# Kernel optimization log

Measured on AMD Instinct MI355X. Metric: run time of the kernel, lower is better.

## Reference

```python
import jax, jax.numpy as jnp
import numpy as np
from jax import lax

B, T1, T2, C = 8, 128, 128, 256
K = 3

def setup_inputs() -> dict:
    key = jax.random.key(0)
    k1, k2, kw, kb = jax.random.split(key, 4)
    x1 = jax.random.normal(k1, (B, T1, C), dtype=jnp.float32)
    x2 = jax.random.normal(k2, (B, T2, C), dtype=jnp.float32)
    # conv2d: in_channels = 2C, out_channels = C, kernel 3x3 (OIHW)
    fan_in = 2 * C * K * K
    bound = 1.0 / np.sqrt(fan_in)
    W = jax.random.uniform(kw, (C, 2 * C, K, K), jnp.float32, -bound, bound)
    b = jax.random.uniform(kb, (C,), jnp.float32, -bound, bound)
    alpha = jnp.float32(0.5)
    return {"x1": x1, "x2": x2, "W": W, "b": b, "alpha": alpha}


def reference(x1, x2, W, b, alpha):
    # x1: [B, T1, C], x2: [B, T2, C]
    a = jnp.transpose(x1, (0, 2, 1))  # [B, C, T1]
    c2 = jnp.transpose(x2, (0, 2, 1))  # [B, C, T2]
    Bd, Cd, T1d = a.shape
    T2d = c2.shape[-1]
    # joint outer-product tensor: [B, 2C, T1, T2]
    j1 = jnp.broadcast_to(a[:, :, :, None], (Bd, Cd, T1d, T2d))
    j2 = jnp.broadcast_to(c2[:, :, None, :], (Bd, Cd, T1d, T2d))
    joint = jnp.concatenate([j1, j2], axis=1)
    out = lax.conv_general_dilated(
        joint, W, window_strides=(1, 1), padding="SAME",
        dimension_numbers=("NCHW", "OIHW", "NCHW"))
    out = out + b[None, :, None, None]
    out = jax.nn.gelu(out, approximate=False)  # torch nn.GELU default = exact erf
    out_T1 = jnp.mean(out, axis=-1)            # [B, C, T1]
    out_T1 = jnp.transpose(out_T1, (0, 2, 1))  # [B, T1, C]
    return out_T1 * alpha + x1
```

## Files before the change

kernel.cpp:

```cpp
#include <hip/hip_runtime.h>
#include <math.h>

#define B_   8
#define T_   128
#define C_   256
#define XLDS 264
#define WLDP 136

typedef unsigned short ushort;
typedef ushort ushort8v __attribute__((ext_vector_type(8)));
typedef __bf16 bf16x8  __attribute__((ext_vector_type(8)));
typedef float  f32x4   __attribute__((ext_vector_type(4)));

__device__ __forceinline__ ushort f2bf(float f) {
    unsigned u = __float_as_uint(f);
    u += 0x7fffu + ((u >> 16) & 1u);
    return (ushort)(u >> 16);
}

__device__ __forceinline__ float gelu_fast(float x) {
    float x2 = x * x;
    float y2 = x * fmaf(-0.10294234f, x2, -2.30220818f);
    float e  = __builtin_amdgcn_exp2f(y2);
    return x * __builtin_amdgcn_rcpf(1.0f + e);
}

__global__ __launch_bounds__(256) void tc_pack(
    const float* __restrict__ x1, const float* __restrict__ x2,
    const float* __restrict__ W, ushort* __restrict__ Xp,
    ushort* __restrict__ Wt)
{
    const int bid = blockIdx.x, t = threadIdx.x;
    if (bid < 256) {
        __shared__ ushort lw[4608];
        const float* src = W + (size_t)bid * 4608;
        #pragma unroll
        for (int i = 0; i < 18; ++i)
            lw[t + i * 256] = f2bf(src[t + i * 256]);
        __syncthreads();
        #pragma unroll
        for (int i = 0; i < 18; ++i) {
            int d  = t + i * 256;
            int s  = d / 2304;
            int e  = d - s * 2304;
            int nj = e / 768;
            int k  = e - nj * 768;
            int sh = k >> 8, ci = k & 255;
            ushort v = (s == 0) ? lw[ci * 9 + sh * 3 + nj]
                                : lw[(256 + ci) * 9 + nj * 3 + sh];
            Wt[((size_t)s * 768 + bid * 3 + nj) * 768 + k] = v;
        }
    } else {
        int g = (bid - 256) * 256 + t;
        int e = g * 8;
        int s  = e >> 18;
        int me = e & 262143;
        const float* src = (s ? x2 : x1) + me;
        float4 lo = *(const float4*)src;
        float4 hi = *(const float4*)(src + 4);
        ushort8v u;
        u[0] = f2bf(lo.x); u[1] = f2bf(lo.y); u[2] = f2bf(lo.z); u[3] = f2bf(lo.w);
        u[4] = f2bf(hi.x); u[5] = f2bf(hi.y); u[6] = f2bf(hi.z); u[7] = f2bf(hi.w);
        *(ushort8v*)&Xp[e] = u;
    }
}

__global__ __launch_bounds__(256, 3) void tc_gemm(
    const ushort* __restrict__ Xp, const ushort* __restrict__ Wt,
    float* __restrict__ AB)
{
    __shared__ ushort Xs[66 * XLDS];
    __shared__ ushort Ws[64 * WLDP];

    const int tn = blockIdx.x;
    const int tm = blockIdx.y;
    const int s  = blockIdx.z;
    const int u  = threadIdx.x;
    const int l  = u & 63, w = u >> 6;
    const int wr = w >> 1, wc = w & 1;
    const int r16 = l & 15, kb = l >> 4;

    const int b_     = tm >> 1;
    const int t_base = (tm & 1) * 64;
    const ushort* Xb = Xp + ((size_t)s * 1024 + b_ * T_) * C_;
    const ushort* Wb = Wt + ((size_t)s * 768 + tn * 64) * 768;

    {
        ushort8v zero = {};
        #pragma unroll
        for (int j = 0; j < 9; ++j) {
            int c = u + j * 256;
            if (j < 8 || c < 2112) {
                int i  = c >> 5;
                int kc = (c & 31) * 8;
                int t  = t_base + i - 1;
                ushort8v v = (t >= 0 && t < T_)
                           ? *(const ushort8v*)(Xb + (size_t)t * C_ + kc) : zero;
                *(ushort8v*)&Xs[i * XLDS + kc] = v;
            }
        }
    }

    ushort8v wbuf[4];
    #pragma unroll
    for (int j = 0; j < 4; ++j) {
        int c = u + j * 256;
        wbuf[j] = *(const ushort8v*)(Wb + (size_t)(c >> 4) * 768 + (c & 15) * 8);
    }

    f32x4 acc[2][2] = {};
    #pragma unroll
    for (int r = 0; r < 6; ++r) {
        const int sh = r >> 1, p = r & 1;
        __syncthreads();
        #pragma unroll
        for (int j = 0; j < 4; ++j) {
            int c = u + j * 256;
            *(ushort8v*)&Ws[(c >> 4) * WLDP + (c & 15) * 8] = wbuf[j];
        }
        if (r < 5) {
            const int rn = r + 1;
            const ushort* wsrc = Wb + (rn >> 1) * 256 + (rn & 1) * 128;
            #pragma unroll
            for (int j = 0; j < 4; ++j) {
                int c = u + j * 256;
                wbuf[j] = *(const ushort8v*)(wsrc + (size_t)(c >> 4) * 768 + (c & 15) * 8);
            }
        }
        __syncthreads();
        #pragma unroll
        for (int ks = 0; ks < 4; ++ks) {
            const int ka = p * 128 + ks * 32 + kb * 8;
            const int kw_ = ks * 32 + kb * 8;
            bf16x8 a0 = __builtin_bit_cast(bf16x8,
                *(const ushort8v*)&Xs[(wr * 32 + r16 + sh) * XLDS + ka]);
            bf16x8 a1 = __builtin_bit_cast(bf16x8,
                *(const ushort8v*)&Xs[(wr * 32 + 16 + r16 + sh) * XLDS + ka]);
            bf16x8 b0 = __builtin_bit_cast(bf16x8,
                *(const ushort8v*)&Ws[(wc * 32 + r16) * WLDP + kw_]);
            bf16x8 b1 = __builtin_bit_cast(bf16x8,
                *(const ushort8v*)&Ws[(wc * 32 + 16 + r16) * WLDP + kw_]);
            acc[0][0] = __builtin_amdgcn_mfma_f32_16x16x32_bf16(a0, b0, acc[0][0], 0, 0, 0);
            acc[0][1] = __builtin_amdgcn_mfma_f32_16x16x32_bf16(a0, b1, acc[0][1], 0, 0, 0);
            acc[1][0] = __builtin_amdgcn_mfma_f32_16x16x32_bf16(a1, b0, acc[1][0], 0, 0, 0);
            acc[1][1] = __builtin_amdgcn_mfma_f32_16x16x32_bf16(a1, b1, acc[1][1], 0, 0, 0);
        }
    }

    #pragma unroll
    for (int j = 0; j < 2; ++j) {
        int n = tn * 64 + wc * 32 + j * 16 + r16;
        #pragma unroll
        for (int i = 0; i < 2; ++i) {
            int m = tm * 64 + wr * 32 + i * 16 + kb * 4;
            *(f32x4*)&AB[((size_t)s * 768 + n) * 1024 + m] = acc[i][j];
        }
    }
}

__global__ __launch_bounds__(128) void tc_fin(
    const float* __restrict__ AB, const float* __restrict__ x1,
    const float* __restrict__ bias, const float* __restrict__ alpha_p,
    float* __restrict__ out)
{
    const int o = blockIdx.x & 255;
    const int b = blockIdx.x >> 8;
    const int t = threadIdx.x;

    __shared__ float Bv[3][T_];

    const float* A0 = AB + ((size_t)o * 3) * 1024 + b * T_ + t;
    const float* A1 = AB + ((size_t)768 + o * 3) * 1024 + b * T_ + t;
    float a0 = A0[0], a1 = A0[1024], a2 = A0[2048];
    float b0 = A1[0], b1 = A1[1024], b2 = A1[2048];

    const float bo = bias[o];
    float A3 = bo + a0 + a1 + a2;
    float Al = bo + a1 + a2;
    float Ar = bo + a0 + a1;
    Bv[0][t] = b0 + b1 + b2;
    Bv[1][t] = b1 + b2;
    Bv[2][t] = b0 + b1;
    __syncthreads();

    int cls = (t == 0) ? 1 : ((t == T_ - 1) ? 2 : 0);
    const float* Bs = Bv[cls];
    float s0 = 0.f, s1 = 0.f, s2 = 0.f, s3 = 0.f;
    for (int j = 0; j < T_; j += 4) {
        f32x4 v = *(const f32x4*)&Bs[j];
        s0 += gelu_fast(A3 + v[0]); s1 += gelu_fast(A3 + v[1]);
        s2 += gelu_fast(A3 + v[2]); s3 += gelu_fast(A3 + v[3]);
    }
    float sm = (s0 + s1) + (s2 + s3);
    float bl = Bs[0], br = Bs[T_ - 1];
    sm += gelu_fast(Al + bl) - gelu_fast(A3 + bl);
    sm += gelu_fast(Ar + br) - gelu_fast(A3 + br);

    const float kk2 = (*alpha_p) * (1.0f / (float)T_);
    size_t go = ((size_t)(b * T_ + t)) * C_ + o;
    out[go] = sm * kk2 + x1[go];
}

extern "C" void kernel_launch(void* const* d_in, const int* in_sizes, int n_in,
                              void* d_out, int out_size, void* d_ws, size_t ws_size,
                              hipStream_t stream) {
    const float* x1    = (const float*)d_in[0];
    const float* x2    = (const float*)d_in[1];
    const float* W     = (const float*)d_in[2];
    const float* bias  = (const float*)d_in[3];
    const float* alpha = (const float*)d_in[4];
    float* out = (float*)d_out;

    float*  AB = (float*)d_ws;
    ushort* Xp = (ushort*)((char*)d_ws + (size_t)2 * 768 * 1024 * 4);
    ushort* Wt = Xp + (size_t)2 * 1024 * 256;

    tc_pack<<<512, 256, 0, stream>>>(x1, x2, W, Xp, Wt);
    tc_gemm<<<dim3(12, 16, 2), 256, 0, stream>>>(Xp, Wt, AB);
    tc_fin<<<B_ * C_, T_, 0, stream>>>(AB, x1, bias, alpha, out);
}
```

Measured before the change: 90.55 us.

## Fuse activation bf16 conversion into GEMM and halve M tile

Removes the separate activation pack pass: the GEMM now reads fp32 x1/x2 directly and converts to bf16 while staging into shared memory, so the bf16 activation buffer is no longer written or read. The M tile shrinks from 64 to 32 rows, which doubles the grid to 768 blocks, halves per-wave accumulators and raises the occupancy hint to 4 blocks per CU. In exchange, each weight tile is loaded by twice as many blocks, there are fewer MFMAs per shared-memory load, and the halo rows make up a larger share of the activation loads.

```diff
diff --git a/kernel.cpp b/kernel.cpp
--- a/kernel.cpp
+++ b/kernel.cpp
@@ -25,51 +25,42 @@
     return x * __builtin_amdgcn_rcpf(1.0f + e);
 }
 
-__global__ __launch_bounds__(256) void tc_pack(
+__device__ __forceinline__ ushort8v pack8(float4 lo, float4 hi) {
+    ushort8v u;
+    u[0] = f2bf(lo.x); u[1] = f2bf(lo.y); u[2] = f2bf(lo.z); u[3] = f2bf(lo.w);
+    u[4] = f2bf(hi.x); u[5] = f2bf(hi.y); u[6] = f2bf(hi.z); u[7] = f2bf(hi.w);
+    return u;
+}
+
+__global__ __launch_bounds__(256) void tc_packw(
+    const float* __restrict__ W, ushort* __restrict__ Wt)
+{
+    const int o = blockIdx.x, t = threadIdx.x;
+    __shared__ ushort lw[4608];
+    const float* src = W + (size_t)o * 4608;
+    #pragma unroll
+    for (int i = 0; i < 18; ++i)
+        lw[t + i * 256] = f2bf(src[t + i * 256]);
+    __syncthreads();
+    #pragma unroll
+    for (int i = 0; i < 18; ++i) {
+        int d  = t + i * 256;
+        int s  = d / 2304;
+        int e  = d - s * 2304;
+        int nj = e / 768;
+        int k  = e - nj * 768;
+        int sh = k >> 8, ci = k & 255;
+        ushort v = (s == 0) ? lw[ci * 9 + sh * 3 + nj]
+                            : lw[(256 + ci) * 9 + nj * 3 + sh];
+        Wt[((size_t)s * 768 + o * 3 + nj) * 768 + k] = v;
+    }
+}
+
+__global__ __launch_bounds__(256, 4) void tc_gemm(
     const float* __restrict__ x1, const float* __restrict__ x2,
-    const float* __restrict__ W, ushort* __restrict__ Xp,
-    ushort* __restrict__ Wt)
+    const ushort* __restrict__ Wt, float* __restrict__ AB)
 {
-    const int bid = blockIdx.x, t = threadIdx.x;
-    if (bid < 256) {
-        __shared__ ushort lw[4608];
-        const float* src = W + (size_t)bid * 4608;
-        #pragma unroll
-        for (int i = 0; i < 18; ++i)
-            lw[t + i * 256] = f2bf(src[t + i * 256]);
-        __syncthreads();
-        #pragma unroll
-        for (int i = 0; i < 18; ++i) {
-            int d  = t + i * 256;
-            int s  = d / 2304;
-            int e  = d - s * 2304;
-            int nj = e / 768;
-            int k  = e - nj * 768;
-            int sh = k >> 8, ci = k & 255;
-            ushort v = (s == 0) ? lw[ci * 9 + sh * 3 + nj]
-                                : lw[(256 + ci) * 9 + nj * 3 + sh];
-            Wt[((size_t)s * 768 + bid * 3 + nj) * 768 + k] = v;
-        }
-    } else {
-        int g = (bid - 256) * 256 + t;
-        int e = g * 8;
-        int s  = e >> 18;
-        int me = e & 262143;
-        const float* src = (s ? x2 : x1) + me;
-        float4 lo = *(const float4*)src;
-        float4 hi = *(const float4*)(src + 4);
-        ushort8v u;
-        u[0] = f2bf(lo.x); u[1] = f2bf(lo.y); u[2] = f2bf(lo.z); u[3] = f2bf(lo.w);
-        u[4] = f2bf(hi.x); u[5] = f2bf(hi.y); u[6] = f2bf(hi.z); u[7] = f2bf(hi.w);
-        *(ushort8v*)&Xp[e] = u;
-    }
-}
-
-__global__ __launch_bounds__(256, 3) void tc_gemm(
-    const ushort* __restrict__ Xp, const ushort* __restrict__ Wt,
-    float* __restrict__ AB)
-{
-    __shared__ ushort Xs[66 * XLDS];
+    __shared__ ushort Xs[34 * XLDS];
     __shared__ ushort Ws[64 * WLDP];
 
     const int tn = blockIdx.x;
@@ -80,22 +71,24 @@
     const int wr = w >> 1, wc = w & 1;
     const int r16 = l & 15, kb = l >> 4;
 
-    const int b_     = tm >> 1;
-    const int t_base = (tm & 1) * 64;
-    const ushort* Xb = Xp + ((size_t)s * 1024 + b_ * T_) * C_;
+    const int b_     = tm >> 2;
+    const int t_base = (tm & 3) * 32;
+    const float*  Xb = (s ? x2 : x1) + (size_t)b_ * T_ * C_;
     const ushort* Wb = Wt + ((size_t)s * 768 + tn * 64) * 768;
 
     {
-        ushort8v zero = {};
         #pragma unroll
-        for (int j = 0; j < 9; ++j) {
+        for (int j = 0; j < 5; ++j) {
             int c = u + j * 256;
-            if (j < 8 || c < 2112) {
+            if (j < 4 || c < 1088) {
                 int i  = c >> 5;
                 int kc = (c & 31) * 8;
                 int t  = t_base + i - 1;
-                ushort8v v = (t >= 0 && t < T_)
-                           ? *(const ushort8v*)(Xb + (size_t)t * C_ + kc) : zero;
+                ushort8v v = {};
+                if (t >= 0 && t < T_) {
+                    const float* p = Xb + (size_t)t * C_ + kc;
+                    v = pack8(*(const float4*)p, *(const float4*)(p + 4));
+                }
                 *(ushort8v*)&Xs[i * XLDS + kc] = v;
             }
         }
@@ -108,7 +101,7 @@
         wbuf[j] = *(const ushort8v*)(Wb + (size_t)(c >> 4) * 768 + (c & 15) * 8);
     }
 
-    f32x4 acc[2][2] = {};
+    f32x4 acc[2] = {};
     #pragma unroll
     for (int r = 0; r < 6; ++r) {
         const int sh = r >> 1, p = r & 1;
@@ -130,31 +123,24 @@
         __syncthreads();
         #pragma unroll
         for (int ks = 0; ks < 4; ++ks) {
-            const int ka = p * 128 + ks * 32 + kb * 8;
+            const int ka  = p * 128 + ks * 32 + kb * 8;
             const int kw_ = ks * 32 + kb * 8;
             bf16x8 a0 = __builtin_bit_cast(bf16x8,
-                *(const ushort8v*)&Xs[(wr * 32 + r16 + sh) * XLDS + ka]);
-            bf16x8 a1 = __builtin_bit_cast(bf16x8,
-                *(const ushort8v*)&Xs[(wr * 32 + 16 + r16 + sh) * XLDS + ka]);
+                *(const ushort8v*)&Xs[(wr * 16 + r16 + sh) * XLDS + ka]);
             bf16x8 b0 = __builtin_bit_cast(bf16x8,
                 *(const ushort8v*)&Ws[(wc * 32 + r16) * WLDP + kw_]);
             bf16x8 b1 = __builtin_bit_cast(bf16x8,
                 *(const ushort8v*)&Ws[(wc * 32 + 16 + r16) * WLDP + kw_]);
-            acc[0][0] = __builtin_amdgcn_mfma_f32_16x16x32_bf16(a0, b0, acc[0][0], 0, 0, 0);
-            acc[0][1] = __builtin_amdgcn_mfma_f32_16x16x32_bf16(a0, b1, acc[0][1], 0, 0, 0);
-            acc[1][0] = __builtin_amdgcn_mfma_f32_16x16x32_bf16(a1, b0, acc[1][0], 0, 0, 0);
-            acc[1][1] = __builtin_amdgcn_mfma_f32_16x16x32_bf16(a1, b1, acc[1][1], 0, 0, 0);
+            acc[0] = __builtin_amdgcn_mfma_f32_16x16x32_bf16(a0, b0, acc[0], 0, 0, 0);
+            acc[1] = __builtin_amdgcn_mfma_f32_16x16x32_bf16(a0, b1, acc[1], 0, 0, 0);
         }
     }
 
     #pragma unroll
     for (int j = 0; j < 2; ++j) {
         int n = tn * 64 + wc * 32 + j * 16 + r16;
-        #pragma unroll
-        for (int i = 0; i < 2; ++i) {
-            int m = tm * 64 + wr * 32 + i * 16 + kb * 4;
-            *(f32x4*)&AB[((size_t)s * 768 + n) * 1024 + m] = acc[i][j];
-        }
+        int m = tm * 32 + wr * 16 + kb * 4;
+        *(f32x4*)&AB[((size_t)s * 768 + n) * 1024 + m] = acc[j];
     }
 }
 
@@ -212,10 +198,9 @@
     float* out = (float*)d_out;
 
     float*  AB = (float*)d_ws;
-    ushort* Xp = (ushort*)((char*)d_ws + (size_t)2 * 768 * 1024 * 4);
-    ushort* Wt = Xp + (size_t)2 * 1024 * 256;
-
-    tc_pack<<<512, 256, 0, stream>>>(x1, x2, W, Xp, Wt);
-    tc_gemm<<<dim3(12, 16, 2), 256, 0, stream>>>(Xp, Wt, AB);
+    ushort* Wt = (ushort*)((char*)d_ws + (size_t)2 * 768 * 1024 * 4);
+
+    tc_packw<<<256, 256, 0, stream>>>(W, Wt);
+    tc_gemm<<<dim3(12, 32, 2), 256, 0, stream>>>(x1, x2, Wt, AB);
     tc_fin<<<B_ * C_, T_, 0, stream>>>(AB, x1, bias, alpha, out);
 }
```

Result: no change. 91.03 us (+0.5%).
